# Kernel optimization log

Hardware: AMD Instinct MI355X
Metric: run time of the kernel (lower is better)

## Reference

```python
import jax, jax.numpy as jnp
import numpy as np

N_NODES = 50000
N_EDGES = 800000
IN_DIM = 256
OUT_DIM = 128
ALPHA = 0.2  # leaky_relu negative slope


def setup_inputs() -> dict:
    key = jax.random.key(0)
    k1, k2, k3, k4, k5 = jax.random.split(key, 5)
    h = jax.random.normal(k1, (N_NODES, IN_DIM), dtype=jnp.float32)
    src = jax.random.randint(k2, (N_EDGES,), 0, N_NODES)
    dst = jax.random.randint(k3, (N_EDGES,), 0, N_NODES)
    W_fc = jax.random.normal(k4, (IN_DIM, OUT_DIM), dtype=jnp.float32) * (1.0 / np.sqrt(IN_DIM))
    attn_w = jax.random.normal(k5, (2 * OUT_DIM,), dtype=jnp.float32) * (1.0 / np.sqrt(2 * OUT_DIM))
    return {"h": h, "src": src, "dst": dst, "W_fc": W_fc, "attn_w": attn_w}


def reference(h, src, dst, W_fc, attn_w):
    n = h.shape[0]
    # fc projection: z = h @ W  -> [N, out]
    z = h @ W_fc
    # edge attention logit: attn_fc(cat(z_src, z_dst)) = z_src@a1 + z_dst@a2
    a1 = attn_w[:OUT_DIM]
    a2 = attn_w[OUT_DIM:]
    logit = z[src] @ a1 + z[dst] @ a2               # [E]
    e = jnp.where(logit >= 0, logit, ALPHA * logit)  # leaky_relu
    # segment softmax over incoming edges of each destination node
    m = jax.ops.segment_max(e, dst, num_segments=n)   # [N], -inf if no edges
    m = jnp.where(jnp.isfinite(m), m, 0.0)
    ex = jnp.exp(e - m[dst])                          # [E]
    denom = jax.ops.segment_sum(ex, dst, num_segments=n)  # [N]
    denom = jnp.where(denom > 0, denom, 1.0)
    alpha_e = ex / denom[dst]                         # [E]
    # weighted scatter-sum of source features
    h_out = jax.ops.segment_sum(alpha_e[:, None] * z[src], dst, num_segments=n)  # [N, out]
    # concat=True -> elu activation
    return jnp.where(h_out > 0, h_out, jnp.expm1(h_out))
```

## Files before the change

kernel.cpp:

```cpp
#include <hip/hip_runtime.h>
#include <math.h>

#define N_NODES 50000
#define N_EDGES 800000
#define IN_DIM 256
#define OUT_DIM 128
#define ALPHA 0.2f

#define BKT 196
#define EPB 4096
#define HIST_NB 196
#define WT_NB   8
#define GEMM_NB 391

typedef __attribute__((ext_vector_type(8))) short short8;
typedef __attribute__((ext_vector_type(4))) float f32x4;

#define OFF_ZB     0u
#define OFF_S1     12800000u
#define OFF_S2     13000000u
#define OFF_OFFS2  13200000u
#define OFF_WT     13400064u
#define OFF_HIST   13465600u
#define OFF_BSTART 13619264u
#define OFF_BCNT   13620048u
#define OFF_TMP    13620832u
#define OFF_SRCS   16820832u

static __device__ __forceinline__ unsigned short f2bf_rne(float f) {
    unsigned int u = __float_as_uint(f);
    unsigned int r = (u + 0x7FFFu + ((u >> 16) & 1u)) >> 16;
    return (unsigned short)r;
}
static __device__ __forceinline__ unsigned int pack2bf(float lo, float hi) {
    return (unsigned int)f2bf_rne(lo) | ((unsigned int)f2bf_rne(hi) << 16);
}

__global__ __launch_bounds__(512) void hist_wt(const int* __restrict__ dst,
                                               const float* __restrict__ W,
                                               int* __restrict__ histT,
                                               unsigned short* __restrict__ WT) {
    __shared__ int hcnt[BKT];
    int b = blockIdx.x, t = threadIdx.x;
    if (b < HIST_NB) {
        for (int i = t; i < BKT; i += 512) hcnt[i] = 0;
        __syncthreads();
#pragma unroll
        for (int q = 0; q < 8; q++) {
            int e = b * EPB + q * 512 + t;
            if (e < N_EDGES) atomicAdd(&hcnt[dst[e] >> 8], 1);
        }
        __syncthreads();
        for (int i = t; i < BKT; i += 512) histT[i * HIST_NB + b] = hcnt[i];
    } else {
        int idx = ((b - HIST_NB) * 512 + t) * 8;
        int c = idx >> 8, k0 = idx & 255;
        unsigned int uu[4];
#pragma unroll
        for (int q = 0; q < 4; q++) {
            float lo = W[(size_t)(k0 + 2 * q) * OUT_DIM + c];
            float hi = W[(size_t)(k0 + 2 * q + 1) * OUT_DIM + c];
            uu[q] = pack2bf(lo, hi);
        }
        *(uint4*)(WT + idx) = make_uint4(uu[0], uu[1], uu[2], uu[3]);
    }
}

__global__ __launch_bounds__(512) void gemm_scatter(const float* __restrict__ h,
                                                    const unsigned short* __restrict__ WT,
                                                    const float* __restrict__ attn,
                                                    unsigned short* __restrict__ zb,
                                                    float* __restrict__ s1,
                                                    float* __restrict__ s2,
                                                    const int* __restrict__ src,
                                                    const int* __restrict__ dst,
                                                    const int* __restrict__ histT,
                                                    unsigned int* __restrict__ tmp,
                                                    int* __restrict__ bstart,
                                                    int* __restrict__ bcnt) {
    __shared__ char smem[32768];
    const int t = threadIdx.x;

    if (blockIdx.x >= GEMM_NB) {
        int m = blockIdx.x - GEMM_NB;
        int* sS      = (int*)smem;
        int* bbL     = sS + 256;
        int* bstartL = bbL + BKT;
        int* cur     = bstartL + BKT;

        int tot = 0, bb = 0;
        if (t < BKT) {
            const int* row = histT + t * HIST_NB;
            for (int m2 = 0; m2 < BKT; m2++) {
                int v = row[m2];
                tot += v;
                bb += (m2 < m) ? v : 0;
            }
            bbL[t] = bb;
            cur[t] = 0;
        }
        int d0 = (t < BKT) ? tot : 0;
        if (t < 256) sS[t] = d0;
        __syncthreads();
        int v = d0;
        for (int ofs = 1; ofs < 256; ofs <<= 1) {
            int add = (t < 256 && t >= ofs) ? sS[t - ofs] : 0;
            __syncthreads();
            if (t < 256) { v += add; sS[t] = v; }
            __syncthreads();
        }
        if (t < BKT) {
            bstartL[t] = v - d0;
            if (m == 0) { bstart[t] = v - d0; bcnt[t] = tot; }
        }
        __syncthreads();

#pragma unroll
        for (int q = 0; q < 8; q++) {
            int e = m * EPB + q * 512 + t;
            if (e < N_EDGES) {
                int d = dst[e];
                int bkt = d >> 8;
                int r = atomicAdd(&cur[bkt], 1);
                tmp[bstartL[bkt] + bbL[bkt] + r] =
                    ((unsigned int)d << 16) | (unsigned int)src[e];
            }
        }
        return;
    }

    const int lane = t & 63, w = t >> 6;
    const int row0 = blockIdx.x * 128;
    const int m16 = lane & 15, kb = lane >> 4;

    const int rA = row0 + w * 16 + m16;
    const float* hrow = h + (size_t)min(rA, N_NODES - 1) * IN_DIM + kb * 8;

    f32x4 acc[8];
#pragma unroll
    for (int ct = 0; ct < 8; ct++) acc[ct] = (f32x4){0.f, 0.f, 0.f, 0.f};

    float4 v0 = *(const float4*)(hrow);
    float4 v1 = *(const float4*)(hrow + 4);

#pragma unroll
    for (int half = 0; half < 2; half++) {
        if (half) __syncthreads();
#pragma unroll
        for (int q = 0; q < 4; q++) {
            int G = t * 4 + q;
            int cc = G >> 4, gs = G & 15;
            const uint4 v = *(const uint4*)(WT + (size_t)cc * IN_DIM + half * 128 + gs * 8);
            *(uint4*)(smem + cc * 256 + ((gs ^ (cc & 7)) * 16)) = v;
        }
        __syncthreads();
#pragma unroll
        for (int kcl = 0; kcl < 4; kcl++) {
            const float4 c0 = v0, c1 = v1;
            int nk = half * 4 + kcl + 1;
            if (nk < 8) {
                v0 = *(const float4*)(hrow + nk * 32);
                v1 = *(const float4*)(hrow + nk * 32 + 4);
            }
            short8 af;
            af[0] = (short)f2bf_rne(c0.x); af[1] = (short)f2bf_rne(c0.y);
            af[2] = (short)f2bf_rne(c0.z); af[3] = (short)f2bf_rne(c0.w);
            af[4] = (short)f2bf_rne(c1.x); af[5] = (short)f2bf_rne(c1.y);
            af[6] = (short)f2bf_rne(c1.z); af[7] = (short)f2bf_rne(c1.w);
            const char* bbase = smem + m16 * 256 + (((kcl * 4 + kb) ^ (m16 & 7)) * 16);
#pragma unroll
            for (int ct = 0; ct < 8; ct++) {
                const short8 bf = *(const short8*)(bbase + ct * 4096);
                acc[ct] = __builtin_amdgcn_mfma_f32_16x16x32_bf16(af, bf, acc[ct], 0, 0, 0);
            }
        }
    }

    float a1v[8], a2v[8];
#pragma unroll
    for (int ct = 0; ct < 8; ct++) {
        a1v[ct] = attn[ct * 16 + m16];
        a2v[ct] = attn[OUT_DIM + ct * 16 + m16];
    }
#pragma unroll
    for (int i = 0; i < 4; i++) {
        int rr = row0 + w * 16 + kb * 4 + i;
        float q1 = 0.f, q2 = 0.f;
#pragma unroll
        for (int ct = 0; ct < 8; ct++) {
            q1 += acc[ct][i] * a1v[ct];
            q2 += acc[ct][i] * a2v[ct];
        }
        q1 += __shfl_xor(q1, 1); q1 += __shfl_xor(q1, 2);
        q1 += __shfl_xor(q1, 4); q1 += __shfl_xor(q1, 8);
        q2 += __shfl_xor(q2, 1); q2 += __shfl_xor(q2, 2);
        q2 += __shfl_xor(q2, 4); q2 += __shfl_xor(q2, 8);
        if (m16 == 0 && rr < N_NODES) { s1[rr] = q1; s2[rr] = q2; }
        if (rr < N_NODES) {
#pragma unroll
            for (int ct = 0; ct < 8; ct++)
                zb[(size_t)rr * OUT_DIM + ct * 16 + m16] = f2bf_rne(acc[ct][i]);
        }
    }
}

__global__ __launch_bounds__(512) void bucket_sort(const unsigned int* __restrict__ tmp,
                                                   const int* __restrict__ bstart,
                                                   const int* __restrict__ bcnt,
                                                   unsigned short* __restrict__ srcs,
                                                   int* __restrict__ offs2) {
    __shared__ int sS[256];
    __shared__ int cnt[256];
    __shared__ int cur[256];
    int t = threadIdx.x, b = blockIdx.x;

    const int myStart = bstart[b];
    const int myCount = bcnt[b];
    if (t < 256) cnt[t] = 0;
    __syncthreads();

    for (int i = t; i < myCount; i += 512)
        atomicAdd(&cnt[(tmp[myStart + i] >> 16) & 255], 1);
    __syncthreads();

    int c0 = 0;
    if (t < 256) { c0 = cnt[t]; sS[t] = c0; }
    __syncthreads();
    int cv = c0;
    for (int ofs = 1; ofs < 256; ofs <<= 1) {
        int add = (t < 256 && t >= ofs) ? sS[t - ofs] : 0;
        __syncthreads();
        if (t < 256) { cv += add; sS[t] = cv; }
        __syncthreads();
    }
    if (t < 256) {
        int excl = cv - c0;
        int node = b * 256 + t;
        if (node < N_NODES) offs2[node] = myStart + excl;
        cur[t] = excl;
    }
    if (b == 0 && t == 0) offs2[N_NODES] = N_EDGES;
    __syncthreads();

    for (int i = t; i < myCount; i += 512) {
        unsigned int u = tmp[myStart + i];
        int r = atomicAdd(&cur[(u >> 16) & 255], 1);
        srcs[myStart + r] = (unsigned short)(u & 0xFFFFu);
    }
}

__global__ __launch_bounds__(256) void aggregate(const unsigned short* __restrict__ zb,
                                                 const int* __restrict__ offs2,
                                                 const unsigned short* __restrict__ srcs,
                                                 const float* __restrict__ s1,
                                                 const float* __restrict__ s2,
                                                 float* __restrict__ out) {
    int wid = (blockIdx.x * blockDim.x + threadIdx.x) >> 6;
    int lane = threadIdx.x & 63;
    if (wid >= N_NODES) return;
    float2* outp = (float2*)(out + (size_t)wid * OUT_DIM) + lane;

    int base = offs2[wid];
    int len = offs2[wid + 1] - base;
    if (len == 0) {
        *outp = make_float2(0.f, 0.f);
        return;
    }
    const float s2v = s2[wid];
    const unsigned int voff = lane * 2;

    float sum = 0.f;
    float ax = 0.f, ay = 0.f;

    for (int c0 = 0; c0 < len; c0 += 64) {
        int i = c0 + lane;
        float ex = 0.f;
        int sj = 0;
        if (i < len) {
            sj = srcs[base + i];
            float lg = s1[sj] + s2v;
            lg = (lg >= 0.f) ? lg : ALPHA * lg;
            ex = __expf(lg);
        }
        sum += ex;
        int cnt = min(64, len - c0);
        int j = 0;
        for (; j + 4 <= cnt; j += 4) {
#pragma unroll
            for (int q = 0; q < 4; q++) {
                int s = __builtin_amdgcn_readlane(sj, j + q);
                float wj = __int_as_float(__builtin_amdgcn_readlane(__float_as_int(ex), j + q));
                unsigned int u = *(const unsigned int*)(zb + (size_t)(unsigned)s * OUT_DIM + voff);
                ax += wj * __uint_as_float(u << 16);
                ay += wj * __uint_as_float(u & 0xFFFF0000u);
            }
        }
        for (; j < cnt; j++) {
            int s = __builtin_amdgcn_readlane(sj, j);
            float wj = __int_as_float(__builtin_amdgcn_readlane(__float_as_int(ex), j));
            unsigned int u = *(const unsigned int*)(zb + (size_t)(unsigned)s * OUT_DIM + voff);
            ax += wj * __uint_as_float(u << 16);
            ay += wj * __uint_as_float(u & 0xFFFF0000u);
        }
    }
#pragma unroll
    for (int m = 32; m >= 1; m >>= 1) sum += __shfl_xor(sum, m);
    float inv = (sum > 0.f) ? 1.f / sum : 1.f;

    float a0 = ax * inv, a1 = ay * inv;
    float2 o;
    o.x = (a0 > 0.f) ? a0 : expm1f(a0);
    o.y = (a1 > 0.f) ? a1 : expm1f(a1);
    *outp = o;
}

extern "C" void kernel_launch(void* const* d_in, const int* in_sizes, int n_in,
                              void* d_out, int out_size, void* d_ws, size_t ws_size,
                              hipStream_t stream) {
    const float* h      = (const float*)d_in[0];
    const int*   src    = (const int*)d_in[1];
    const int*   dst    = (const int*)d_in[2];
    const float* W_fc   = (const float*)d_in[3];
    const float* attn_w = (const float*)d_in[4];
    float* out = (float*)d_out;

    char* ws = (char*)d_ws;
    unsigned short* zb = (unsigned short*)(ws + OFF_ZB);
    float* s1       = (float*)(ws + OFF_S1);
    float* s2       = (float*)(ws + OFF_S2);
    int*   offs2    = (int*)(ws + OFF_OFFS2);
    unsigned short* WT = (unsigned short*)(ws + OFF_WT);
    int*   histT    = (int*)(ws + OFF_HIST);
    int*   bstart   = (int*)(ws + OFF_BSTART);
    int*   bcnt     = (int*)(ws + OFF_BCNT);
    unsigned int* tmp = (unsigned int*)(ws + OFF_TMP);
    unsigned short* srcs = (unsigned short*)(ws + OFF_SRCS);

    hist_wt<<<HIST_NB + WT_NB, 512, 0, stream>>>(dst, W_fc, histT, WT);
    gemm_scatter<<<GEMM_NB + HIST_NB, 512, 0, stream>>>(h, WT, attn_w, zb, s1, s2,
                                                        src, dst, histT, tmp, bstart, bcnt);
    bucket_sort<<<BKT, 512, 0, stream>>>(tmp, bstart, bcnt, srcs, offs2);
    aggregate<<<(N_NODES * 64) / 256, 256, 0, stream>>>(zb, offs2, srcs, s1, s2, out);
}
```

Baseline: 77.20 us.

## Precompute per-bucket column prefix sums in a separate scan kernel

Adds a small colscan kernel that turns the per-block bucket histogram into exclusive prefix offsets and bucket totals once. Before, each of the 196 scatter blocks looped serially over 196 histogram entries per bucket. Scatter blocks now load their base offset and totals directly, and bucket_sort recomputes its bucket start from the totals with a shared-memory scan. This removes redundant serial work inside gemm_scatter at the cost of one extra kernel launch and a scan repeated in every bucket_sort block.

```diff
diff --git a/kernel.cpp b/kernel.cpp
--- a/kernel.cpp
+++ b/kernel.cpp
@@ -22,10 +22,10 @@
 #define OFF_OFFS2  13200000u
 #define OFF_WT     13400064u
 #define OFF_HIST   13465600u
-#define OFF_BSTART 13619264u
-#define OFF_BCNT   13620048u
-#define OFF_TMP    13620832u
-#define OFF_SRCS   16820832u
+#define OFF_BBT    13619264u
+#define OFF_BTOT   13772928u
+#define OFF_TMP    13773952u
+#define OFF_SRCS   16973952u
 
 static __device__ __forceinline__ unsigned short f2bf_rne(float f) {
     unsigned int u = __float_as_uint(f);
@@ -66,6 +66,26 @@
     }
 }
 
+__global__ __launch_bounds__(256) void colscan(const int* __restrict__ histT,
+                                               int* __restrict__ bbaseT,
+                                               int* __restrict__ btot) {
+    __shared__ int s[256];
+    int t = threadIdx.x, b = blockIdx.x;
+    int d0 = (t < HIST_NB) ? histT[b * HIST_NB + t] : 0;
+    s[t] = d0;
+    __syncthreads();
+    int v = d0;
+    for (int ofs = 1; ofs < 256; ofs <<= 1) {
+        int add = (t >= ofs) ? s[t - ofs] : 0;
+        __syncthreads();
+        v += add;
+        s[t] = v;
+        __syncthreads();
+    }
+    if (t < HIST_NB) bbaseT[b * HIST_NB + t] = v - d0;
+    if (t == HIST_NB - 1) btot[b] = v;
+}
+
 __global__ __launch_bounds__(512) void gemm_scatter(const float* __restrict__ h,
                                                     const unsigned short* __restrict__ WT,
                                                     const float* __restrict__ attn,
@@ -74,10 +94,9 @@
                                                     float* __restrict__ s2,
                                                     const int* __restrict__ src,
                                                     const int* __restrict__ dst,
-                                                    const int* __restrict__ histT,
-                                                    unsigned int* __restrict__ tmp,
-                                                    int* __restrict__ bstart,
-                                                    int* __restrict__ bcnt) {
+                                                    const int* __restrict__ bbaseT,
+                                                    const int* __restrict__ btot,
+                                                    unsigned int* __restrict__ tmp) {
     __shared__ char smem[32768];
     const int t = threadIdx.x;
 
@@ -88,18 +107,8 @@
         int* bstartL = bbL + BKT;
         int* cur     = bstartL + BKT;
 
-        int tot = 0, bb = 0;
-        if (t < BKT) {
-            const int* row = histT + t * HIST_NB;
-            for (int m2 = 0; m2 < BKT; m2++) {
-                int v = row[m2];
-                tot += v;
-                bb += (m2 < m) ? v : 0;
-            }
-            bbL[t] = bb;
-            cur[t] = 0;
-        }
-        int d0 = (t < BKT) ? tot : 0;
+        if (t < BKT) { bbL[t] = bbaseT[t * HIST_NB + m]; cur[t] = 0; }
+        int d0 = (t < BKT) ? btot[t] : 0;
         if (t < 256) sS[t] = d0;
         __syncthreads();
         int v = d0;
@@ -109,10 +118,7 @@
             if (t < 256) { v += add; sS[t] = v; }
             __syncthreads();
         }
-        if (t < BKT) {
-            bstartL[t] = v - d0;
-            if (m == 0) { bstart[t] = v - d0; bcnt[t] = tot; }
-        }
+        if (t < BKT) bstartL[t] = v - d0;
         __syncthreads();
 
 #pragma unroll
@@ -205,19 +211,28 @@
 }
 
 __global__ __launch_bounds__(512) void bucket_sort(const unsigned int* __restrict__ tmp,
-                                                   const int* __restrict__ bstart,
-                                                   const int* __restrict__ bcnt,
+                                                   const int* __restrict__ btot,
                                                    unsigned short* __restrict__ srcs,
                                                    int* __restrict__ offs2) {
     __shared__ int sS[256];
     __shared__ int cnt[256];
     __shared__ int cur[256];
+    __shared__ int msS, mcS;
     int t = threadIdx.x, b = blockIdx.x;
 
-    const int myStart = bstart[b];
-    const int myCount = bcnt[b];
-    if (t < 256) cnt[t] = 0;
-    __syncthreads();
+    int d0 = (t < BKT) ? btot[t] : 0;
+    if (t < 256) { sS[t] = d0; cnt[t] = 0; }
+    __syncthreads();
+    int v = d0;
+    for (int ofs = 1; ofs < 256; ofs <<= 1) {
+        int add = (t < 256 && t >= ofs) ? sS[t - ofs] : 0;
+        __syncthreads();
+        if (t < 256) { v += add; sS[t] = v; }
+        __syncthreads();
+    }
+    if (t == b) { msS = v - d0; mcS = d0; }
+    __syncthreads();
+    const int myStart = msS, myCount = mcS;
 
     for (int i = t; i < myCount; i += 512)
         atomicAdd(&cnt[(tmp[myStart + i] >> 16) & 255], 1);
@@ -331,14 +346,15 @@
     int*   offs2    = (int*)(ws + OFF_OFFS2);
     unsigned short* WT = (unsigned short*)(ws + OFF_WT);
     int*   histT    = (int*)(ws + OFF_HIST);
-    int*   bstart   = (int*)(ws + OFF_BSTART);
-    int*   bcnt     = (int*)(ws + OFF_BCNT);
+    int*   bbaseT   = (int*)(ws + OFF_BBT);
+    int*   btot     = (int*)(ws + OFF_BTOT);
     unsigned int* tmp = (unsigned int*)(ws + OFF_TMP);
     unsigned short* srcs = (unsigned short*)(ws + OFF_SRCS);
 
     hist_wt<<<HIST_NB + WT_NB, 512, 0, stream>>>(dst, W_fc, histT, WT);
+    colscan<<<BKT, 256, 0, stream>>>(histT, bbaseT, btot);
     gemm_scatter<<<GEMM_NB + HIST_NB, 512, 0, stream>>>(h, WT, attn_w, zb, s1, s2,
-                                                        src, dst, histT, tmp, bstart, bcnt);
-    bucket_sort<<<BKT, 512, 0, stream>>>(tmp, bstart, bcnt, srcs, offs2);
+                                                        src, dst, bbaseT, btot, tmp);
+    bucket_sort<<<BKT, 512, 0, stream>>>(tmp, btot, srcs, offs2);
     aggregate<<<(N_NODES * 64) / 256, 256, 0, stream>>>(zb, offs2, srcs, s1, s2, out);
 }
```

Result: no change. 76.23 us (-1.3%).
